# Optimization experiments

Hardware: AMD Instinct MI355X
Metric: run time of the kernel (lower is better)

Reference implementation:

```python
import jax, jax.numpy as jnp
import numpy as np

N_HEAD = 16
N_KV_HEAD = 4
N_EMBD = 2048

def rotate_half(x):
    x1, x2 = jnp.split(x, 2, axis=-1)
    return jnp.concatenate([-x2, x1], axis=-1)

def rope_tables(T, k):
    # angles = 10000^(-2*i/k) for i in [0, k/2); cos/sin repeated twice along last dim
    inv = jnp.power(10000.0, -2.0 * jnp.arange(k // 2, dtype=jnp.float32) / k)
    ang = jnp.arange(T, dtype=jnp.float32)[:, None] * inv[None, :]  # [T, k/2]
    cos = jnp.tile(jnp.cos(ang), (1, 2))  # [T, k]
    sin = jnp.tile(jnp.sin(ang), (1, 2))
    return cos, sin

def setup_inputs() -> dict:
    key = jax.random.key(0)
    ks = jax.random.split(key, 5)
    B, T, D = 4, 1024, N_EMBD
    g, h = N_KV_HEAD, N_HEAD
    k = D // h
    s = 0.02
    return {
        'x': jax.random.normal(ks[0], (B, T, D), dtype=jnp.float32),
        'Wq': jax.random.normal(ks[1], (D, D), dtype=jnp.float32) * s,
        'Wk': jax.random.normal(ks[2], (D, g * k), dtype=jnp.float32) * s,
        'Wv': jax.random.normal(ks[3], (D, g * k), dtype=jnp.float32) * s,
        'Wo': jax.random.normal(ks[4], (D, D), dtype=jnp.float32) * s,
    }

def reference(x, Wq, Wk, Wv, Wo):
    B, T, D = x.shape
    h, g = N_HEAD, N_KV_HEAD
    k = D // h
    Q = (x @ Wq).reshape(B, T, h, k).transpose(0, 2, 1, 3)  # [B,h,T,k]
    K = (x @ Wk).reshape(B, T, g, k).transpose(0, 2, 1, 3)  # [B,g,T,k]
    V = (x @ Wv).reshape(B, T, g, k).transpose(0, 2, 1, 3)
    # GQA: repeat_interleave kv heads to match query heads
    K = jnp.repeat(K, h // g, axis=1)  # [B,h,T,k]
    V = jnp.repeat(V, h // g, axis=1)
    cos, sin = rope_tables(T, k)
    cos = cos[None, None]  # [1,1,T,k]
    sin = sin[None, None]
    Q = Q * cos + rotate_half(Q) * sin
    K = K * cos + rotate_half(K) * sin
    scores = jnp.einsum('bhqk,bhsk->bhqs', Q, K) / jnp.sqrt(jnp.float32(k))
    causal = jnp.tril(jnp.ones((T, T), dtype=bool))
    scores = jnp.where(causal[None, None], scores, -jnp.inf)
    A = jax.nn.softmax(scores, axis=-1)
    Y = jnp.einsum('bhqs,bhsk->bhqk', A, V)
    Y = Y.transpose(0, 2, 1, 3).reshape(B, T, D)
    return Y @ Wo
```

## Files before the change

kernel.cpp:

```cpp
#include <hip/hip_runtime.h>
#include <math.h>

#define B_ 4
#define T_ 1024
#define D_ 2048
#define NH 16
#define NKV 4
#define HD 128
#define KV_D 512
#define QKV_S 2560

typedef __attribute__((ext_vector_type(8))) short short8;
typedef __attribute__((ext_vector_type(4))) float f32x4;

__device__ __forceinline__ ushort f2b(float f) {
    unsigned u = __float_as_uint(f);
    return (ushort)((u + 0x7fffu + ((u >> 16) & 1u)) >> 16);
}
__device__ __forceinline__ float b2f(ushort u) {
    return __uint_as_float((unsigned)u << 16);
}

#if __has_builtin(__builtin_amdgcn_exp2f)
#define EXP2F(x) __builtin_amdgcn_exp2f(x)
#else
#define EXP2F(x) __expf((x) * 0.6931471805599453f)
#endif

#define ASYNC_COPY16(g, l)                                                  \
    __builtin_amdgcn_global_load_lds(                                       \
        (const __attribute__((address_space(1))) void*)(g),                 \
        (__attribute__((address_space(3))) void*)(l), 16, 0, 0)

#define SBAR()                                                              \
    do {                                                                    \
        __builtin_amdgcn_sched_barrier(0);                                  \
        asm volatile("" ::: "memory");                                      \
        __builtin_amdgcn_s_barrier();                                       \
        asm volatile("" ::: "memory");                                      \
        __builtin_amdgcn_sched_barrier(0);                                  \
    } while (0)
#define WAITV(n) asm volatile("s_waitcnt vmcnt(" #n ")" ::: "memory")
#define LGKM0()                                                             \
    do {                                                                    \
        asm volatile("s_waitcnt lgkmcnt(0)" ::: "memory");                  \
        __builtin_amdgcn_sched_barrier(0);                                  \
    } while (0)
#define MFMA16(ap, bp, cc) cc = __builtin_amdgcn_mfma_f32_16x16x32_bf16(ap, bp, cc, 0, 0, 0)

__global__ __launch_bounds__(256) void prep_all(const float* __restrict__ x,
                                                const float* __restrict__ Wq,
                                                const float* __restrict__ Wk,
                                                const float* __restrict__ Wv,
                                                const float* __restrict__ Wo,
                                                ushort* __restrict__ xb,
                                                ushort* __restrict__ WqkvT,
                                                ushort* __restrict__ WoT,
                                                float2* __restrict__ tab) {
    __shared__ float tile[32][33];
    const int bid = blockIdx.x;
    if (bid < 8192) {
        const int i = bid * 256 + threadIdx.x;
        const float4 v = ((const float4*)x)[i];
        ushort4 u;
        u.x = f2b(v.x); u.y = f2b(v.y); u.z = f2b(v.z); u.w = f2b(v.w);
        ((ushort4*)xb)[i] = u;
        return;
    }
    if (bid >= 18432) {
        const int idx = (bid - 18432) * 256 + threadIdx.x;
        const int t = idx >> 6, i = idx & 63;
        const float inv = exp2f((float)i * (-13.287712379549449f / 64.0f));
        const float ang = (float)t * inv;
        tab[idx] = make_float2(cosf(ang), sinf(ang));
        return;
    }
    const float* W;
    ushort* WT;
    int N, rb;
    if (bid < 12288)      { W = Wq; WT = WqkvT;                           N = D_;   rb = bid - 8192; }
    else if (bid < 13312) { W = Wk; WT = WqkvT + (size_t)D_ * D_;         N = KV_D; rb = bid - 12288; }
    else if (bid < 14336) { W = Wv; WT = WqkvT + (size_t)(D_+KV_D) * D_;  N = KV_D; rb = bid - 13312; }
    else                  { W = Wo; WT = WoT;                             N = D_;   rb = bid - 14336; }
    const int bxn = N / 32;
    const int n0 = (rb % bxn) * 32, k0 = (rb / bxn) * 32;
    const int tx = threadIdx.x & 31, ty = threadIdx.x >> 5;
    for (int i = ty; i < 32; i += 8)
        tile[i][tx] = W[(size_t)(k0 + i) * N + n0 + tx];
    __syncthreads();
    for (int i = ty; i < 32; i += 8)
        WT[(size_t)(n0 + i) * D_ + k0 + tx] = f2b(tile[tx][i]);
}

__global__ __launch_bounds__(512, 2) void gemm_qkv256(const ushort* __restrict__ A,
                                                      const ushort* __restrict__ BT,
                                                      ushort* __restrict__ QKV,
                                                      ushort* __restrict__ Vt,
                                                      const float2* __restrict__ tab) {
    extern __shared__ ushort smem[];
    const int K = D_;
    const int NT = K / 64;
    const int tid = threadIdx.x;
    const int m0 = blockIdx.y * 256, n0 = blockIdx.x * 256;
    const int wave = tid >> 6, lane = tid & 63;
    const int wr = wave >> 2, wc = wave & 3;
    const int ln = lane & 15, quad = lane >> 4;

    const int rl = tid >> 3;
    const int cu = (tid & 7) * 8;
    const int cus = cu ^ ((rl & 1) << 5);
    const ushort* Ag = A + (size_t)(m0 + rl) * K + cus;
    const ushort* Bg = BT + (size_t)(n0 + rl) * K + cus;
    ushort* const Asl = smem;
    ushort* const stA = Asl + tid * 8;
    ushort* const stB = smem + 32768 + tid * 8;

    const int kse = (ln & 1) << 5;
    const int afrag0 = wr * 8192 + ln * 64 + quad * 8;
    const int bfrag0 = 32768 + (wc >> 1) * 8192 + ((wc & 1) * 64 + ln) * 64 + quad * 8;

    f32x4 acc[8][4];
    const f32x4 zero = {0.f, 0.f, 0.f, 0.f};
#pragma unroll
    for (int i = 0; i < 8; ++i)
#pragma unroll
        for (int j = 0; j < 4; ++j) acc[i][j] = zero;

#pragma unroll
    for (int h = 0; h < 2; ++h)
#pragma unroll
        for (int i = 0; i < 2; ++i)
            ASYNC_COPY16(Ag + (size_t)(h * 128 + i * 64) * K, stA + h * 8192 + i * 4096);
#pragma unroll
    for (int h = 0; h < 2; ++h)
#pragma unroll
        for (int i = 0; i < 2; ++i)
            ASYNC_COPY16(Bg + (size_t)(h * 128 + i * 64) * K, stB + h * 8192 + i * 4096);

    for (int t = 0; t < NT; ++t) {
        const int d = t & 1;
        const int db = d * 16384;
        const int dn = (d ^ 1) * 16384;
        const ushort* Agk = Ag + (t + 1) * 64;
        const ushort* Bgk = Bg + (t + 1) * 64;
        if (t + 1 < NT) {
#pragma unroll
            for (int h = 0; h < 2; ++h)
#pragma unroll
                for (int i = 0; i < 2; ++i)
                    ASYNC_COPY16(Agk + (size_t)(h * 128 + i * 64) * K,
                                 stA + dn + h * 8192 + i * 4096);
            WAITV(4);
        } else {
            WAITV(0);
        }
        SBAR();

        short8 a[4][2], b0[2][2], b1[2][2];
        const ushort* Ah = Asl + db + afrag0;
        const ushort* Bh = smem + db + bfrag0;

#pragma unroll
        for (int mt = 0; mt < 4; ++mt) {
            a[mt][0] = *(const short8*)(Ah + mt * 1024 + (0 ^ kse));
            a[mt][1] = *(const short8*)(Ah + mt * 1024 + (32 ^ kse));
        }
#pragma unroll
        for (int nt = 0; nt < 2; ++nt) {
            b0[nt][0] = *(const short8*)(Bh + nt * 1024 + (0 ^ kse));
            b0[nt][1] = *(const short8*)(Bh + nt * 1024 + (32 ^ kse));
        }
        if (t + 1 < NT) {
            ASYNC_COPY16(Bgk, stB + dn);
            ASYNC_COPY16(Bgk + (size_t)64 * K, stB + dn + 4096);
        }
        SBAR();
        LGKM0();
        __builtin_amdgcn_s_setprio(1);
#pragma unroll
        for (int mt = 0; mt < 4; ++mt)
#pragma unroll
            for (int nt = 0; nt < 2; ++nt) {
                MFMA16(a[mt][0], b0[nt][0], acc[mt][nt]);
                MFMA16(a[mt][1], b0[nt][1], acc[mt][nt]);
            }
        __builtin_amdgcn_s_setprio(0);
        SBAR();

#pragma unroll
        for (int nt = 0; nt < 2; ++nt) {
            b1[nt][0] = *(const short8*)(Bh + 2048 + nt * 1024 + (0 ^ kse));
            b1[nt][1] = *(const short8*)(Bh + 2048 + nt * 1024 + (32 ^ kse));
        }
        if (t + 1 < NT) {
            ASYNC_COPY16(Bgk + (size_t)128 * K, stB + dn + 8192);
            ASYNC_COPY16(Bgk + (size_t)192 * K, stB + dn + 12288);
        }
        SBAR();
        LGKM0();
        __builtin_amdgcn_s_setprio(1);
#pragma unroll
        for (int mt = 0; mt < 4; ++mt)
#pragma unroll
            for (int nt = 0; nt < 2; ++nt) {
                MFMA16(a[mt][0], b1[nt][0], acc[mt][2 + nt]);
                MFMA16(a[mt][1], b1[nt][1], acc[mt][2 + nt]);
            }
        __builtin_amdgcn_s_setprio(0);
        SBAR();

#pragma unroll
        for (int mt = 0; mt < 4; ++mt) {
            a[mt][0] = *(const short8*)(Ah + 4096 + mt * 1024 + (0 ^ kse));
            a[mt][1] = *(const short8*)(Ah + 4096 + mt * 1024 + (32 ^ kse));
        }
        SBAR();
        LGKM0();
        __builtin_amdgcn_s_setprio(1);
#pragma unroll
        for (int mt = 0; mt < 4; ++mt)
#pragma unroll
            for (int nt = 0; nt < 2; ++nt) {
                MFMA16(a[mt][0], b1[nt][0], acc[4 + mt][2 + nt]);
                MFMA16(a[mt][1], b1[nt][1], acc[4 + mt][2 + nt]);
            }
        __builtin_amdgcn_s_setprio(0);
        SBAR();

        SBAR();
        LGKM0();
        __builtin_amdgcn_s_setprio(1);
#pragma unroll
        for (int mt = 0; mt < 4; ++mt)
#pragma unroll
            for (int nt = 0; nt < 2; ++nt) {
                MFMA16(a[mt][0], b0[nt][0], acc[4 + mt][nt]);
                MFMA16(a[mt][1], b0[nt][1], acc[4 + mt][nt]);
            }
        __builtin_amdgcn_s_setprio(0);
        SBAR();
    }

    __syncthreads();
    ushort* Epi = smem;
    const int b = m0 >> 10;
    const int t0 = m0 & 1023;
    const int hid0 = n0 >> 7;

    for (int hh = 0; hh < 2; ++hh) {
        if ((wc >> 1) == hh) {
            const int cb = (wc & 1) * 64;
#pragma unroll
            for (int am = 0; am < 8; ++am)
#pragma unroll
                for (int an = 0; an < 4; ++an)
#pragma unroll
                    for (int r = 0; r < 4; ++r)
                        Epi[(wr * 128 + am * 16 + quad * 4 + r) * 136 + cb + an * 16 + ln] =
                            f2b(acc[am][an][r]);
        }
        __syncthreads();

        const int hid = hid0 + hh;
        if (hid < NH + NKV) {
            const bool isQ = hid < NH;
            const size_t colbase = isQ ? (size_t)hid * HD : (size_t)D_ + (size_t)(hid - NH) * HD;
            const float sc = isQ ? (0.08838834764831845f * 1.4426950408889634f) : 1.0f;
            const int r = tid >> 1;
            const int hf = tid & 1;
            const int tt = t0 + r;
            ushort* orow = QKV + (size_t)(m0 + r) * QKV_S + colbase;
            const float4* tab4 = (const float4*)tab;
#pragma unroll
            for (int jj = 0; jj < 4; ++jj) {
                const int dbase = hf * 32 + jj * 8;
                const short8 lo = *(const short8*)&Epi[r * 136 + dbase];
                const short8 hi = *(const short8*)&Epi[r * 136 + 64 + dbase];
                ushort olo[8], ohi[8];
#pragma unroll
                for (int kq = 0; kq < 4; ++kq) {
                    const float4 cs = tab4[((tt * 64 + dbase) >> 1) + kq];
                    const float x1a = b2f(lo[2 * kq]),     x2a = b2f(hi[2 * kq]);
                    const float x1b = b2f(lo[2 * kq + 1]), x2b = b2f(hi[2 * kq + 1]);
                    olo[2 * kq]     = f2b((x1a * cs.x - x2a * cs.y) * sc);
                    ohi[2 * kq]     = f2b((x2a * cs.x + x1a * cs.y) * sc);
                    olo[2 * kq + 1] = f2b((x1b * cs.z - x2b * cs.w) * sc);
                    ohi[2 * kq + 1] = f2b((x2b * cs.z + x1b * cs.w) * sc);
                }
                *(short8*)&orow[dbase]      = *(short8*)olo;
                *(short8*)&orow[dbase + 64] = *(short8*)ohi;
            }
        } else {
            const int kv = hid - (NH + NKV);
            const int dd = tid & 127;
            const int th = tid >> 7;
            ushort* vrow = Vt + ((size_t)((b * NKV + kv) * HD + dd)) * T_ + t0 + th * 64;
#pragma unroll
            for (int jj = 0; jj < 8; ++jj) {
                ushort pk[8];
#pragma unroll
                for (int k2 = 0; k2 < 8; ++k2)
                    pk[k2] = Epi[(th * 64 + jj * 8 + k2) * 136 + dd];
                *(short8*)&vrow[jj * 8] = *(short8*)pk;
            }
        }
        __syncthreads();
    }
}

__global__ __launch_bounds__(256) void gemm_bf16(const ushort* __restrict__ A,
                                                 const ushort* __restrict__ BT,
                                                 float* __restrict__ C,
                                                 int M, int N, int K) {
    __shared__ ushort As[128 * 32];
    __shared__ ushort Bs[128 * 32];
    const int tid = threadIdx.x;
    const int m0 = blockIdx.y * 128, n0 = blockIdx.x * 128;
    const int wave = tid >> 6, lane = tid & 63;
    const int wm = (wave >> 1) * 64, wn = (wave & 1) * 64;
    const int lrow = lane & 15;
    const int quad = lane >> 4;

    f32x4 acc[4][4];
    const f32x4 zero = {0.f, 0.f, 0.f, 0.f};
#pragma unroll
    for (int i = 0; i < 4; ++i)
#pragma unroll
        for (int j = 0; j < 4; ++j) acc[i][j] = zero;

    const int srow = tid >> 2;
    const int scol = (tid & 3) * 8;
    const ushort* Ag = A + (size_t)(m0 + srow) * K + scol;
    const ushort* Bg = BT + (size_t)(n0 + srow) * K + scol;
    ushort* AsT = As + tid * 8;
    ushort* BsT = Bs + tid * 8;

    for (int k0 = 0; k0 < K; k0 += 32) {
        ASYNC_COPY16(Ag + k0, AsT);
        ASYNC_COPY16(Ag + k0 + (size_t)64 * K, AsT + 64 * 32);
        ASYNC_COPY16(Bg + k0, BsT);
        ASYNC_COPY16(Bg + k0 + (size_t)64 * K, BsT + 64 * 32);
        __syncthreads();

        short8 a[4], b[4];
#pragma unroll
        for (int mt = 0; mt < 4; ++mt)
            a[mt] = *(const short8*)&As[(wm + mt * 16 + lrow) * 32 + quad * 8];
#pragma unroll
        for (int nt = 0; nt < 4; ++nt)
            b[nt] = *(const short8*)&Bs[(wn + nt * 16 + lrow) * 32 + quad * 8];
#pragma unroll
        for (int mt = 0; mt < 4; ++mt)
#pragma unroll
            for (int nt = 0; nt < 4; ++nt)
                acc[mt][nt] = __builtin_amdgcn_mfma_f32_16x16x32_bf16(
                    a[mt], b[nt], acc[mt][nt], 0, 0, 0);
        __syncthreads();
    }

    const int crow = quad * 4;
    const int ccol = lrow;
#pragma unroll
    for (int mt = 0; mt < 4; ++mt)
#pragma unroll
        for (int nt = 0; nt < 4; ++nt)
#pragma unroll
            for (int r = 0; r < 4; ++r)
                C[(size_t)(m0 + wm + mt * 16 + crow + r) * N +
                  n0 + wn + nt * 16 + ccol] = acc[mt][nt][r];
}

__global__ __launch_bounds__(256) void attn_mfma(const ushort* __restrict__ QKV,
                                                 const ushort* __restrict__ Vt,
                                                 ushort* __restrict__ Yb) {
    __shared__ ushort Ks[64][136];
    __shared__ ushort Vs[128][72];
    __shared__ ushort Ps[4][16][72];

    const int bh = blockIdx.x;
    const int qt = (int)gridDim.y - 1 - (int)blockIdx.y;
    const int b = bh >> 4, h = bh & 15;
    const int kvh = h >> 2;
    const int q0 = qt * 64;
    const int tid = threadIdx.x;
    const int wave = tid >> 6, lane = tid & 63;
    const int ln = lane & 15, quad = lane >> 4;

    short8 qf[4];
    {
        const ushort* qp = QKV + ((size_t)(b * T_ + q0 + wave * 16 + ln)) * QKV_S + h * HD + quad * 8;
#pragma unroll
        for (int f = 0; f < 4; ++f) qf[f] = *(const short8*)(qp + f * 32);
    }

    f32x4 acc[8];
    const f32x4 zero = {0.f, 0.f, 0.f, 0.f};
#pragma unroll
    for (int j = 0; j < 8; ++j) acc[j] = zero;
    float m_r[4], l_r[4];
#pragma unroll
    for (int r = 0; r < 4; ++r) { m_r[r] = -INFINITY; l_r[r] = 0.f; }

    const int qrow = q0 + wave * 16 + quad * 4;

    for (int kt = 0; kt <= qt; ++kt) {
        const int s0 = kt * 64;
        __syncthreads();
#pragma unroll
        for (int c = 0; c < 4; ++c) {
            const int cid = tid + 256 * c;
            const int s = cid >> 4, ch = cid & 15;
            *(short8*)&Ks[s][ch * 8] =
                *(const short8*)&QKV[((size_t)(b * T_ + s0 + s)) * QKV_S + D_ + kvh * HD + ch * 8];
        }
#pragma unroll
        for (int c = 0; c < 4; ++c) {
            const int cid = tid + 256 * c;
            const int d = cid >> 3, ch = cid & 7;
            *(short8*)&Vs[d][ch * 8] =
                *(const short8*)&Vt[((size_t)((b * NKV + kvh) * HD + d)) * T_ + s0 + ch * 8];
        }
        __syncthreads();

        float sc[4][4];
#pragma unroll
        for (int ct = 0; ct < 4; ++ct) {
            f32x4 s4 = zero;
#pragma unroll
            for (int f = 0; f < 4; ++f)
                s4 = __builtin_amdgcn_mfma_f32_16x16x32_bf16(
                    qf[f], *(const short8*)&Ks[ct * 16 + ln][f * 32 + quad * 8], s4, 0, 0, 0);
#pragma unroll
            for (int r = 0; r < 4; ++r) sc[ct][r] = s4[r];
        }
        if (kt == qt) {
#pragma unroll
            for (int ct = 0; ct < 4; ++ct)
#pragma unroll
                for (int r = 0; r < 4; ++r)
                    if (s0 + ct * 16 + ln > qrow + r) sc[ct][r] = -INFINITY;
        }
        float alpha[4];
#pragma unroll
        for (int r = 0; r < 4; ++r) {
            float mx = fmaxf(fmaxf(sc[0][r], sc[1][r]), fmaxf(sc[2][r], sc[3][r]));
            mx = fmaxf(mx, __shfl_xor(mx, 1));
            mx = fmaxf(mx, __shfl_xor(mx, 2));
            mx = fmaxf(mx, __shfl_xor(mx, 4));
            mx = fmaxf(mx, __shfl_xor(mx, 8));
            const float mnew = fmaxf(m_r[r], mx);
            alpha[r] = EXP2F(m_r[r] - mnew);
            m_r[r] = mnew;
#pragma unroll
            for (int ct = 0; ct < 4; ++ct) sc[ct][r] = EXP2F(sc[ct][r] - mnew);
            float sum = (sc[0][r] + sc[1][r]) + (sc[2][r] + sc[3][r]);
            sum += __shfl_xor(sum, 1);
            sum += __shfl_xor(sum, 2);
            sum += __shfl_xor(sum, 4);
            sum += __shfl_xor(sum, 8);
            l_r[r] = l_r[r] * alpha[r] + sum;
        }
#pragma unroll
        for (int ct = 0; ct < 4; ++ct)
#pragma unroll
            for (int r = 0; r < 4; ++r)
                Ps[wave][quad * 4 + r][ct * 16 + ln] = f2b(sc[ct][r]);
#pragma unroll
        for (int j = 0; j < 8; ++j)
#pragma unroll
            for (int r = 0; r < 4; ++r) acc[j][r] *= alpha[r];
        const short8 pa0 = *(const short8*)&Ps[wave][ln][quad * 8];
        const short8 pa1 = *(const short8*)&Ps[wave][ln][32 + quad * 8];
#pragma unroll
        for (int j = 0; j < 8; ++j) {
            acc[j] = __builtin_amdgcn_mfma_f32_16x16x32_bf16(
                pa0, *(const short8*)&Vs[j * 16 + ln][quad * 8], acc[j], 0, 0, 0);
            acc[j] = __builtin_amdgcn_mfma_f32_16x16x32_bf16(
                pa1, *(const short8*)&Vs[j * 16 + ln][32 + quad * 8], acc[j], 0, 0, 0);
        }
    }

    float invl[4];
#pragma unroll
    for (int r = 0; r < 4; ++r) invl[r] = 1.f / l_r[r];
    ushort* yb = Yb + ((size_t)(b * T_ + qrow)) * D_ + h * HD + ln;
#pragma unroll
    for (int r = 0; r < 4; ++r)
#pragma unroll
        for (int j = 0; j < 8; ++j)
            yb[(size_t)r * D_ + j * 16] = f2b(acc[j][r] * invl[r]);
}

extern "C" void kernel_launch(void* const* d_in, const int* in_sizes, int n_in,
                              void* d_out, int out_size, void* d_ws, size_t ws_size,
                              hipStream_t stream) {
    const float* x  = (const float*)d_in[0];
    const float* Wq = (const float*)d_in[1];
    const float* Wk = (const float*)d_in[2];
    const float* Wv = (const float*)d_in[3];
    const float* Wo = (const float*)d_in[4];
    float* out = (float*)d_out;

    char* w = (char*)d_ws;
    ushort* xb    = (ushort*)w;  w += (size_t)4096 * D_ * 2;
    ushort* WqkvT = (ushort*)w;  w += (size_t)3072 * D_ * 2;
    ushort* QKV   = (ushort*)w;  w += (size_t)4096 * QKV_S * 2;
    ushort* Vt    = (ushort*)w;  w += (size_t)B_ * KV_D * T_ * 2;
    ushort* Yb    = (ushort*)w;  w += (size_t)4096 * D_ * 2;
    ushort* WoT   = (ushort*)w;  w += (size_t)D_ * D_ * 2;
    float2* tab   = (float2*)w;  w += (size_t)T_ * 64 * 8;

    const int M = B_ * T_;
    dim3 blk(256);

    hipFuncSetAttribute(reinterpret_cast<const void*>(gemm_qkv256),
                        hipFuncAttributeMaxDynamicSharedMemorySize, 131072);

    prep_all<<<18688, blk, 0, stream>>>(x, Wq, Wk, Wv, Wo, xb, WqkvT, WoT, tab);

    gemm_qkv256<<<dim3(3072 / 256, M / 256), dim3(512), 131072, stream>>>(xb, WqkvT, QKV, Vt, tab);

    attn_mfma<<<dim3(B_ * NH, T_ / 64), blk, 0, stream>>>(QKV, Vt, Yb);

    gemm_bf16<<<dim3(D_ / 128, M / 128), blk, 0, stream>>>(Yb, WoT, out, M, D_, D_);
}
```

Baseline: 321.3 us.

## Restructure QKV GEMM main loop with prefetched fragments and 8-way LDS swizzle

The K-loop of the QKV projection GEMM is reorganized. Next-tile A/B fragments are now read from LDS at the end of the previous iteration, and all global-to-LDS async copies are issued at the top of each iteration. Explicit lgkmcnt waits are gone and there are fewer barriers per iteration. The LDS swizzle changes from a 1-bit XOR on alternate rows to an 8-row XOR pattern, meant to cut bank conflicts on fragment reads. The risk is relying on compiler-inserted waits and fewer barriers for correctness of the double-buffer reuse.

```diff
diff --git a/kernel.cpp b/kernel.cpp
--- a/kernel.cpp
+++ b/kernel.cpp
@@ -32,20 +32,9 @@
         (const __attribute__((address_space(1))) void*)(g),                 \
         (__attribute__((address_space(3))) void*)(l), 16, 0, 0)
 
-#define SBAR()                                                              \
-    do {                                                                    \
-        __builtin_amdgcn_sched_barrier(0);                                  \
-        asm volatile("" ::: "memory");                                      \
-        __builtin_amdgcn_s_barrier();                                       \
-        asm volatile("" ::: "memory");                                      \
-        __builtin_amdgcn_sched_barrier(0);                                  \
-    } while (0)
-#define WAITV(n) asm volatile("s_waitcnt vmcnt(" #n ")" ::: "memory")
-#define LGKM0()                                                             \
-    do {                                                                    \
-        asm volatile("s_waitcnt lgkmcnt(0)" ::: "memory");                  \
-        __builtin_amdgcn_sched_barrier(0);                                  \
-    } while (0)
+#define SCHED0() __builtin_amdgcn_sched_barrier(0)
+#define SBAR() __builtin_amdgcn_s_barrier()
+#define WAITV0() asm volatile("s_waitcnt vmcnt(0)" ::: "memory")
 #define MFMA16(ap, bp, cc) cc = __builtin_amdgcn_mfma_f32_16x16x32_bf16(ap, bp, cc, 0, 0, 0)
 
 __global__ __launch_bounds__(256) void prep_all(const float* __restrict__ x,
@@ -107,17 +96,15 @@
     const int ln = lane & 15, quad = lane >> 4;
 
     const int rl = tid >> 3;
-    const int cu = (tid & 7) * 8;
-    const int cus = cu ^ ((rl & 1) << 5);
+    const int cus = ((tid & 7) * 8) ^ ((rl & 7) << 3);
     const ushort* Ag = A + (size_t)(m0 + rl) * K + cus;
     const ushort* Bg = BT + (size_t)(n0 + rl) * K + cus;
-    ushort* const Asl = smem;
-    ushort* const stA = Asl + tid * 8;
+    ushort* const stA = smem + tid * 8;
     ushort* const stB = smem + 32768 + tid * 8;
 
-    const int kse = (ln & 1) << 5;
-    const int afrag0 = wr * 8192 + ln * 64 + quad * 8;
-    const int bfrag0 = 32768 + (wc >> 1) * 8192 + ((wc & 1) * 64 + ln) * 64 + quad * 8;
+    const int cq0 = (quad * 8) ^ ((ln & 7) << 3);
+    const int abase0 = wr * 8192 + ln * 64;
+    const int bbase0 = 32768 + (wc >> 1) * 8192 + ((wc & 1) * 64 + ln) * 64;
 
     f32x4 acc[8][4];
     const f32x4 zero = {0.f, 0.f, 0.f, 0.f};
@@ -126,120 +113,91 @@
 #pragma unroll
         for (int j = 0; j < 4; ++j) acc[i][j] = zero;
 
-#pragma unroll
-    for (int h = 0; h < 2; ++h)
-#pragma unroll
-        for (int i = 0; i < 2; ++i)
-            ASYNC_COPY16(Ag + (size_t)(h * 128 + i * 64) * K, stA + h * 8192 + i * 4096);
-#pragma unroll
-    for (int h = 0; h < 2; ++h)
-#pragma unroll
-        for (int i = 0; i < 2; ++i)
-            ASYNC_COPY16(Bg + (size_t)(h * 128 + i * 64) * K, stB + h * 8192 + i * 4096);
-
+    short8 a[4][2], b0[2][2], b1[2][2];
+
+#define GLOADS(dnoff, koff)                                                 \
+    do {                                                                    \
+        const ushort* Agk = Ag + (koff);                                    \
+        const ushort* Bgk = Bg + (koff);                                    \
+        ASYNC_COPY16(Agk,                    stA + (dnoff));                \
+        ASYNC_COPY16(Agk + (size_t)64 * K,   stA + (dnoff) + 4096);         \
+        ASYNC_COPY16(Agk + (size_t)128 * K,  stA + (dnoff) + 8192);         \
+        ASYNC_COPY16(Agk + (size_t)192 * K,  stA + (dnoff) + 12288);        \
+        ASYNC_COPY16(Bgk,                    stB + (dnoff));                \
+        ASYNC_COPY16(Bgk + (size_t)64 * K,   stB + (dnoff) + 4096);         \
+        ASYNC_COPY16(Bgk + (size_t)128 * K,  stB + (dnoff) + 8192);         \
+        ASYNC_COPY16(Bgk + (size_t)192 * K,  stB + (dnoff) + 12288);        \
+    } while (0)
+
+#define READ_A(dst, base, roff)                                             \
+    _Pragma("unroll")                                                       \
+    for (int mt = 0; mt < 4; ++mt) {                                        \
+        dst[mt][0] = *(const short8*)&smem[(base) + (roff) + mt * 1024 + cq0];        \
+        dst[mt][1] = *(const short8*)&smem[(base) + (roff) + mt * 1024 + (cq0 ^ 32)]; \
+    }
+#define READ_B(dst, base, noff)                                             \
+    _Pragma("unroll")                                                       \
+    for (int nt = 0; nt < 2; ++nt) {                                        \
+        dst[nt][0] = *(const short8*)&smem[(base) + (noff) + nt * 1024 + cq0];        \
+        dst[nt][1] = *(const short8*)&smem[(base) + (noff) + nt * 1024 + (cq0 ^ 32)]; \
+    }
+#define QUAD_MMA(ar, br, mo, no)                                            \
+    _Pragma("unroll")                                                       \
+    for (int mt = 0; mt < 4; ++mt)                                          \
+        _Pragma("unroll")                                                   \
+        for (int nt = 0; nt < 2; ++nt) {                                    \
+            MFMA16(ar[mt][0], br[nt][0], acc[(mo) + mt][(no) + nt]);        \
+            MFMA16(ar[mt][1], br[nt][1], acc[(mo) + mt][(no) + nt]);        \
+        }
+
+    GLOADS(0, 0);
+    WAITV0();
+    SBAR();
+    SCHED0();
+    READ_A(a, abase0, 0);
+    READ_B(b0, bbase0, 0);
+
+#pragma unroll 1
     for (int t = 0; t < NT; ++t) {
-        const int d = t & 1;
-        const int db = d * 16384;
-        const int dn = (d ^ 1) * 16384;
-        const ushort* Agk = Ag + (t + 1) * 64;
-        const ushort* Bgk = Bg + (t + 1) * 64;
-        if (t + 1 < NT) {
-#pragma unroll
-            for (int h = 0; h < 2; ++h)
-#pragma unroll
-                for (int i = 0; i < 2; ++i)
-                    ASYNC_COPY16(Agk + (size_t)(h * 128 + i * 64) * K,
-                                 stA + dn + h * 8192 + i * 4096);
-            WAITV(4);
-        } else {
-            WAITV(0);
-        }
+        const int cb = (t & 1) * 16384;
+        const int nb = cb ^ 16384;
+        const bool more = (t + 1) < NT;
+
+        READ_B(b1, bbase0 + cb, 2048);
+        if (more) GLOADS(nb, (t + 1) * 64);
+        SCHED0();
         SBAR();
-
-        short8 a[4][2], b0[2][2], b1[2][2];
-        const ushort* Ah = Asl + db + afrag0;
-        const ushort* Bh = smem + db + bfrag0;
-
-#pragma unroll
-        for (int mt = 0; mt < 4; ++mt) {
-            a[mt][0] = *(const short8*)(Ah + mt * 1024 + (0 ^ kse));
-            a[mt][1] = *(const short8*)(Ah + mt * 1024 + (32 ^ kse));
-        }
-#pragma unroll
-        for (int nt = 0; nt < 2; ++nt) {
-            b0[nt][0] = *(const short8*)(Bh + nt * 1024 + (0 ^ kse));
-            b0[nt][1] = *(const short8*)(Bh + nt * 1024 + (32 ^ kse));
-        }
-        if (t + 1 < NT) {
-            ASYNC_COPY16(Bgk, stB + dn);
-            ASYNC_COPY16(Bgk + (size_t)64 * K, stB + dn + 4096);
-        }
+        __builtin_amdgcn_s_setprio(1);
+        QUAD_MMA(a, b0, 0, 0);
+        __builtin_amdgcn_s_setprio(0);
+
+        SCHED0();
         SBAR();
-        LGKM0();
         __builtin_amdgcn_s_setprio(1);
-#pragma unroll
-        for (int mt = 0; mt < 4; ++mt)
-#pragma unroll
-            for (int nt = 0; nt < 2; ++nt) {
-                MFMA16(a[mt][0], b0[nt][0], acc[mt][nt]);
-                MFMA16(a[mt][1], b0[nt][1], acc[mt][nt]);
-            }
+        QUAD_MMA(a, b1, 0, 2);
         __builtin_amdgcn_s_setprio(0);
+
+        READ_A(a, abase0 + cb, 4096);
+        __builtin_amdgcn_s_setprio(1);
+        QUAD_MMA(a, b1, 4, 2);
+        __builtin_amdgcn_s_setprio(0);
+
+        if (more) WAITV0();
+        SCHED0();
         SBAR();
-
-#pragma unroll
-        for (int nt = 0; nt < 2; ++nt) {
-            b1[nt][0] = *(const short8*)(Bh + 2048 + nt * 1024 + (0 ^ kse));
-            b1[nt][1] = *(const short8*)(Bh + 2048 + nt * 1024 + (32 ^ kse));
-        }
-        if (t + 1 < NT) {
-            ASYNC_COPY16(Bgk + (size_t)128 * K, stB + dn + 8192);
-            ASYNC_COPY16(Bgk + (size_t)192 * K, stB + dn + 12288);
-        }
-        SBAR();
-        LGKM0();
+        SCHED0();
         __builtin_amdgcn_s_setprio(1);
-#pragma unroll
-        for (int mt = 0; mt < 4; ++mt)
-#pragma unroll
-            for (int nt = 0; nt < 2; ++nt) {
-                MFMA16(a[mt][0], b1[nt][0], acc[mt][2 + nt]);
-                MFMA16(a[mt][1], b1[nt][1], acc[mt][2 + nt]);
-            }
+        QUAD_MMA(a, b0, 4, 0);
         __builtin_amdgcn_s_setprio(0);
-        SBAR();
-
-#pragma unroll
-        for (int mt = 0; mt < 4; ++mt) {
-            a[mt][0] = *(const short8*)(Ah + 4096 + mt * 1024 + (0 ^ kse));
-            a[mt][1] = *(const short8*)(Ah + 4096 + mt * 1024 + (32 ^ kse));
-        }
-        SBAR();
-        LGKM0();
-        __builtin_amdgcn_s_setprio(1);
-#pragma unroll
-        for (int mt = 0; mt < 4; ++mt)
-#pragma unroll
-            for (int nt = 0; nt < 2; ++nt) {
-                MFMA16(a[mt][0], b1[nt][0], acc[4 + mt][2 + nt]);
-                MFMA16(a[mt][1], b1[nt][1], acc[4 + mt][2 + nt]);
-            }
-        __builtin_amdgcn_s_setprio(0);
-        SBAR();
-
-        SBAR();
-        LGKM0();
-        __builtin_amdgcn_s_setprio(1);
-#pragma unroll
-        for (int mt = 0; mt < 4; ++mt)
-#pragma unroll
-            for (int nt = 0; nt < 2; ++nt) {
-                MFMA16(a[mt][0], b0[nt][0], acc[4 + mt][nt]);
-                MFMA16(a[mt][1], b0[nt][1], acc[4 + mt][nt]);
-            }
-        __builtin_amdgcn_s_setprio(0);
-        SBAR();
-    }
+        if (more) {
+            READ_A(a, abase0 + nb, 0);
+            READ_B(b0, bbase0 + nb, 0);
+        }
+    }
+#undef GLOADS
+#undef READ_A
+#undef READ_B
+#undef QUAD_MMA
 
     __syncthreads();
     ushort* Epi = smem;
@@ -249,14 +207,14 @@
 
     for (int hh = 0; hh < 2; ++hh) {
         if ((wc >> 1) == hh) {
-            const int cb = (wc & 1) * 64;
+            const int cb2 = (wc & 1) * 64;
 #pragma unroll
             for (int am = 0; am < 8; ++am)
 #pragma unroll
                 for (int an = 0; an < 4; ++an)
 #pragma unroll
                     for (int r = 0; r < 4; ++r)
-                        Epi[(wr * 128 + am * 16 + quad * 4 + r) * 136 + cb + an * 16 + ln] =
+                        Epi[(wr * 128 + am * 16 + quad * 4 + r) * 136 + cb2 + an * 16 + ln] =
                             f2b(acc[am][an][r]);
         }
         __syncthreads();
```

New measurement: 302.5 us. -5.9%, faster.
